# Optimization experiments

Measured on AMD Instinct MI355X. Metric: run time of the kernel, lower is better.

Reference implementation:

```python
import jax, jax.numpy as jnp
import numpy as np

SEQ = 4096
STATE_DIM = 512
ACTION_DIM = 496
T_DIM = 16
EMBED = STATE_DIM + ACTION_DIM + T_DIM  # 1024
HEADS = 4
HEAD_DIM = EMBED // HEADS
FF = 4096
N_EXP = 8
TOP_K = 2
EPS = 1e-5


def _ln(x, g, b):
    m = jnp.mean(x, -1, keepdims=True)
    v = jnp.var(x, -1, keepdims=True)
    return (x - m) * jax.lax.rsqrt(v + EPS) * g + b


def setup_inputs() -> dict:
    key = jax.random.key(0)
    ks = jax.random.split(key, 24)
    s = lambda k, shape, scale=0.02: jax.random.normal(k, shape, dtype=jnp.float32) * scale
    return {
        "x": jax.random.normal(ks[0], (SEQ, ACTION_DIM), dtype=jnp.float32),
        "time": jax.random.randint(ks[1], (SEQ,), 0, 6),
        "state": jax.random.normal(ks[2], (SEQ, 1, STATE_DIM), dtype=jnp.float32),
        "time_table": s(ks[3], (6, T_DIM), 1.0),
        "expert_w": s(ks[4], (N_EXP, EMBED, EMBED)),   # [n, in, out]
        "expert_b": jnp.zeros((N_EXP, EMBED), jnp.float32),
        "gate_w": s(ks[5], (EMBED, N_EXP)),
        "gate_b": jnp.zeros((N_EXP,), jnp.float32),
        "in_proj_w": s(ks[6], (EMBED, 3 * EMBED)),
        "in_proj_b": jnp.zeros((3 * EMBED,), jnp.float32),
        "out_proj_w": s(ks[7], (EMBED, EMBED)),
        "out_proj_b": jnp.zeros((EMBED,), jnp.float32),
        "ln1_g": jnp.ones((EMBED,), jnp.float32),
        "ln1_b": jnp.zeros((EMBED,), jnp.float32),
        "ff1_w": s(ks[8], (EMBED, FF)),
        "ff1_b": jnp.zeros((FF,), jnp.float32),
        "ff2_w": s(ks[9], (FF, ACTION_DIM)),
        "ff2_b": jnp.zeros((ACTION_DIM,), jnp.float32),
        "ln2_g": jnp.ones((ACTION_DIM,), jnp.float32),
        "ln2_b": jnp.zeros((ACTION_DIM,), jnp.float32),
    }


def reference(x, time, state, time_table, expert_w, expert_b, gate_w, gate_b,
              in_proj_w, in_proj_b, out_proj_w, out_proj_b,
              ln1_g, ln1_b, ff1_w, ff1_b, ff2_w, ff2_b, ln2_g, ln2_b):
    # combine inputs -> [S, EMBED]
    t_emb = time_table[time]                      # [S, t_dim]
    h = jnp.concatenate([x, t_emb, state[:, 0, :]], axis=-1)

    # MoE: softmax gate, top-k combine over densely-computed expert outputs
    gate = jax.nn.softmax(h @ gate_w + gate_b, axis=-1)      # [S, N]
    scores, idx = jax.lax.top_k(gate, TOP_K)                 # [S, K]
    all_out = jnp.einsum('se,nef->snf', h, expert_w) + expert_b[None]  # [S, N, E]
    comb = jnp.zeros_like(gate).at[jnp.arange(SEQ)[:, None], idx].add(scores)
    moe = jnp.einsum('sn,snf->sf', comb, all_out)            # [S, E]

    # multi-head self-attention (torch nn.MultiheadAttention, unbatched)
    qkv = moe @ in_proj_w + in_proj_b
    q, k, v = jnp.split(qkv, 3, axis=-1)
    q = q.reshape(SEQ, HEADS, HEAD_DIM) * (HEAD_DIM ** -0.5)
    k = k.reshape(SEQ, HEADS, HEAD_DIM)
    v = v.reshape(SEQ, HEADS, HEAD_DIM)
    att = jax.nn.softmax(jnp.einsum('shd,thd->hst', q, k), axis=-1)
    ao = jnp.einsum('hst,thd->shd', att, v).reshape(SEQ, EMBED)
    ao = ao @ out_proj_w + out_proj_b

    out1 = _ln(moe + ao, ln1_g, ln1_b)
    ff = jax.nn.relu(out1 @ ff1_w + ff1_b) @ ff2_w + ff2_b   # [S, action_dim]
    return _ln(ff, ln2_g, ln2_b)
```

## Files before the change

kernel.cpp:

```cpp
#include <hip/hip_runtime.h>
#include <hip/hip_bf16.h>

typedef __hip_bfloat16 hb;
typedef __bf16 bf16x8 __attribute__((ext_vector_type(8)));
typedef float f32x4 __attribute__((ext_vector_type(4)));

#define SEQ 4096
#define EMBED 1024
#define NHEAD 4
#define HDIM 256
#define FFD 4096
#define NEXP 8
#define ADIM 496
#define NSLOT 9216

static __device__ __forceinline__ float b2f(hb x) { return __bfloat162float(x); }
static __device__ __forceinline__ hb f2b(float x) { return __float2bfloat16(x); }

#define GLOAD_LDS16(g, l)                                                      \
  __builtin_amdgcn_global_load_lds(                                            \
      (const __attribute__((address_space(1))) void*)(g),                      \
      (__attribute__((address_space(3))) void*)(l), 16, 0, 0)

#define GEMM_KLOOP64(KMAX)                                                     \
  for (int kt = 0; kt < (KMAX); kt += 64) {                                    \
    GLOAD_LDS16(Ag + kt, sA + wave * 512);                                     \
    GLOAD_LDS16(Ag + kt + 32, sA + 4096 + wave * 512);                         \
    GLOAD_LDS16(Ag + kt + 64 * lda_, sA + 2048 + wave * 512);                  \
    GLOAD_LDS16(Ag + kt + 64 * lda_ + 32, sA + 6144 + wave * 512);             \
    GLOAD_LDS16(Bg + kt, sB + wave * 512);                                     \
    GLOAD_LDS16(Bg + kt + 32, sB + 4096 + wave * 512);                         \
    GLOAD_LDS16(Bg + kt + 64 * ldb_, sB + 2048 + wave * 512);                  \
    GLOAD_LDS16(Bg + kt + 64 * ldb_ + 32, sB + 6144 + wave * 512);             \
    __syncthreads();                                                           \
    _Pragma("unroll") for (int ks = 0; ks < 2; ks++) {                         \
      bf16x8 av[4], bv[4];                                                     \
      _Pragma("unroll") for (int i = 0; i < 4; i++) {                          \
        const int row = wr * 64 + i * 16 + lm;                                 \
        av[i] = *(const bf16x8*)&sA[ks * 4096 + row * 32 + sw8];               \
      }                                                                        \
      _Pragma("unroll") for (int i = 0; i < 4; i++) {                          \
        const int row = wc * 64 + i * 16 + lm;                                 \
        bv[i] = *(const bf16x8*)&sB[ks * 4096 + row * 32 + sw8];               \
      }                                                                        \
      _Pragma("unroll") for (int i = 0; i < 4; i++)                            \
          _Pragma("unroll") for (int j = 0; j < 4; j++) acc[i][j] =            \
          __builtin_amdgcn_mfma_f32_16x16x32_bf16(av[i], bv[j], acc[i][j], 0,  \
                                                  0, 0);                       \
    }                                                                          \
    __syncthreads();                                                           \
  }

#define GEMM_PROLOGUE                                                          \
  const int m0 = blockIdx.y * 128, n0 = blockIdx.x * 128;                      \
  const int tid = threadIdx.x;                                                 \
  const int wave = tid >> 6, lane = tid & 63;                                  \
  const int quad = lane >> 4, lm = lane & 15;                                  \
  const int wr = wave >> 1, wc = wave & 1;                                     \
  const int r0 = tid >> 2;                                                     \
  const int cg = 8 * ((tid & 3) ^ ((tid >> 2) & 3));                           \
  const int sw8 = (quad ^ (lm & 3)) * 8;

#define EPILOGUE_B16(DST, LDC)                                                 \
  {                                                                            \
    hb* eb = smem + wave * 1024;                                               \
    _Pragma("unroll") for (int i = 0; i < 4; i++) {                            \
      _Pragma("unroll") for (int j = 0; j < 4; j++) {                          \
        const int c = ((j ^ quad) << 4) + lm;                                  \
        _Pragma("unroll") for (int rr = 0; rr < 4; rr++)                       \
            eb[(quad * 4 + rr) * 64 + c] = f2b(acc[i][j][rr]);                 \
      }                                                                        \
      _Pragma("unroll") for (int p = 0; p < 2; p++) {                          \
        const int r = p * 8 + (lane >> 3);                                     \
        const int cgc = lane & 7;                                              \
        const int gs = (cgc >> 1) ^ (r >> 2);                                  \
        const bf16x8 val =                                                     \
            *(const bf16x8*)&eb[r * 64 + gs * 16 + (cgc & 1) * 8];             \
        const long grow = m0 + wr * 64 + i * 16 + r;                           \
        *(bf16x8*)&DST[grow * (LDC) + n0 + wc * 64 + cgc * 8] = val;           \
      }                                                                        \
    }                                                                          \
  }

__global__ __launch_bounds__(256) void gemm_bt(
    const hb* __restrict__ A, long lda, long bA,
    const hb* __restrict__ B, long ldb, long bB,
    hb* __restrict__ C, long ldc, long bC,
    int K, const float* __restrict__ bias, int relu) {
  __shared__ __align__(16) hb smem[2 * 128 * 64];
  hb* sA = smem;
  hb* sB = smem + 8192;
  const int z = blockIdx.z;
  A += (long)z * bA;
  B += (long)z * bB;
  C += (long)z * bC;
  GEMM_PROLOGUE
  const long lda_ = lda, ldb_ = ldb;
  const hb* Ag = A + (long)(m0 + r0) * lda + cg;
  const hb* Bg = B + (long)(n0 + r0) * ldb + cg;

  f32x4 acc[4][4] = {};
  GEMM_KLOOP64(K)

  hb* eb = smem + wave * 1024;
#pragma unroll
  for (int i = 0; i < 4; i++) {
#pragma unroll
    for (int j = 0; j < 4; j++) {
      const float bval = bias ? bias[n0 + wc * 64 + j * 16 + lm] : 0.f;
      const int c = ((j ^ quad) << 4) + lm;
#pragma unroll
      for (int rr = 0; rr < 4; rr++) {
        float v = acc[i][j][rr] + bval;
        if (relu) v = fmaxf(v, 0.f);
        eb[(quad * 4 + rr) * 64 + c] = f2b(v);
      }
    }
#pragma unroll
    for (int p = 0; p < 2; p++) {
      const int r = p * 8 + (lane >> 3);
      const int cgc = lane & 7;
      const int gs = (cgc >> 1) ^ (r >> 2);
      const bf16x8 val = *(const bf16x8*)&eb[r * 64 + gs * 16 + (cgc & 1) * 8];
      const long grow = m0 + wr * 64 + i * 16 + r;
      *(bf16x8*)&C[grow * ldc + n0 + wc * 64 + cgc * 8] = val;
    }
  }
}

__global__ __launch_bounds__(256) void gemm_bt_exp(
    const hb* __restrict__ A, long lda, long bA,
    const hb* __restrict__ B, long ldb, long bB,
    hb* __restrict__ C, long ldc, long bC,
    int K, float scale, hb* __restrict__ rsP) {
  __shared__ __align__(16) hb smem[2 * 128 * 64];
  hb* sA = smem;
  hb* sB = smem + 8192;
  const int z = blockIdx.z;
  A += (long)z * bA;
  B += (long)z * bB;
  C += (long)z * bC;
  GEMM_PROLOGUE
  const long lda_ = lda, ldb_ = ldb;
  const hb* Ag = A + (long)(m0 + r0) * lda + cg;
  const hb* Bg = B + (long)(n0 + r0) * ldb + cg;

  f32x4 acc[4][4] = {};
  GEMM_KLOOP64(K)

  hb* eb = smem + wave * 1024;
  float* rbuf = (float*)sB;
  float rs[4][4];
#pragma unroll
  for (int i = 0; i < 4; i++) {
    float r4[4] = {0.f, 0.f, 0.f, 0.f};
#pragma unroll
    for (int j = 0; j < 4; j++) {
      const int c = ((j ^ quad) << 4) + lm;
#pragma unroll
      for (int rr = 0; rr < 4; rr++) {
        const float e = __expf(acc[i][j][rr] * scale);
        r4[rr] += e;
        eb[(quad * 4 + rr) * 64 + c] = f2b(e);
      }
    }
#pragma unroll
    for (int rr = 0; rr < 4; rr++) {
      r4[rr] += __shfl_xor(r4[rr], 1);
      r4[rr] += __shfl_xor(r4[rr], 2);
      r4[rr] += __shfl_xor(r4[rr], 4);
      r4[rr] += __shfl_xor(r4[rr], 8);
      rs[i][rr] = r4[rr];
    }
#pragma unroll
    for (int p = 0; p < 2; p++) {
      const int r = p * 8 + (lane >> 3);
      const int cgc = lane & 7;
      const int gs = (cgc >> 1) ^ (r >> 2);
      const bf16x8 val = *(const bf16x8*)&eb[r * 64 + gs * 16 + (cgc & 1) * 8];
      const long grow = m0 + wr * 64 + i * 16 + r;
      *(bf16x8*)&C[grow * ldc + n0 + wc * 64 + cgc * 8] = val;
    }
  }
  if (lm == 0) {
#pragma unroll
    for (int i = 0; i < 4; i++)
#pragma unroll
      for (int rr = 0; rr < 4; rr++)
        rbuf[(wr * 2 + wc) * 64 + i * 16 + quad * 4 + rr] = rs[i][rr];
  }
  __syncthreads();
  if (tid < 128) {
    const int lwr = tid >> 6, r64 = tid & 63;
    const float d = rbuf[lwr * 128 + r64] + rbuf[lwr * 128 + 64 + r64];
    rsP[((long)blockIdx.x * gridDim.z + z) * SEQ + m0 + lwr * 64 + r64] =
        f2b(d);
  }
}

__global__ __launch_bounds__(256) void gemm_bt_splitk(
    const hb* __restrict__ A, long lda, long bA,
    const hb* __restrict__ B, long ldb, long bB,
    float* __restrict__ Cp, int ldcp, long pstride, int Ksub, int shift) {
  const int z = blockIdx.z;
  const int batch = z >> shift, split = z - (batch << shift);
  A += (long)batch * bA + (long)split * Ksub;
  B += (long)batch * bB + (long)split * Ksub;
  Cp += (long)z * pstride;
  __shared__ __align__(16) hb smem[2 * 128 * 64];
  hb* sA = smem;
  hb* sB = smem + 8192;
  GEMM_PROLOGUE
  const long lda_ = lda, ldb_ = ldb;
  const hb* Ag = A + (long)(m0 + r0) * lda + cg;
  const hb* Bg = B + (long)(n0 + r0) * ldb + cg;

  f32x4 acc[4][4] = {};
  GEMM_KLOOP64(Ksub)

  float* ef = (float*)smem + wave * 1024;
#pragma unroll
  for (int i = 0; i < 4; i++) {
#pragma unroll
    for (int j = 0; j < 4; j++) {
      const int c = ((j ^ quad) << 4) + lm;
#pragma unroll
      for (int rr = 0; rr < 4; rr++)
        ef[(quad * 4 + rr) * 64 + c] = acc[i][j][rr];
    }
#pragma unroll
    for (int p = 0; p < 4; p++) {
      const int r = p * 4 + (lane >> 4);
      const int cgc = lane & 15;
      const int gs = (cgc >> 2) ^ (r >> 2);
      const f32x4 val = *(const f32x4*)&ef[r * 64 + gs * 16 + (cgc & 3) * 4];
      const long grow = m0 + wr * 64 + i * 16 + r;
      *(f32x4*)&Cp[grow * ldcp + n0 + wc * 64 + cgc * 4] = val;
    }
  }
}

__global__ __launch_bounds__(256) void gemm_bt_splitk_b16(
    const hb* __restrict__ A, long lda, long bA,
    const hb* __restrict__ B, long ldb, long bB,
    hb* __restrict__ Cp, int ldcp, long pstride, int Ksub, int shift) {
  const int z = blockIdx.z;
  const int batch = z >> shift, split = z - (batch << shift);
  A += (long)batch * bA + (long)split * Ksub;
  B += (long)batch * bB + (long)split * Ksub;
  Cp += (long)z * pstride;
  __shared__ __align__(16) hb smem[2 * 128 * 64];
  hb* sA = smem;
  hb* sB = smem + 8192;
  GEMM_PROLOGUE
  const long lda_ = lda, ldb_ = ldb;
  const hb* Ag = A + (long)(m0 + r0) * lda + cg;
  const hb* Bg = B + (long)(n0 + r0) * ldb + cg;

  f32x4 acc[4][4] = {};
  GEMM_KLOOP64(Ksub)
  EPILOGUE_B16(Cp, ldcp)
}

__global__ __launch_bounds__(256) void reduce_splitk(
    const float* __restrict__ part, long pstride, int nsplit, int shift,
    hb* __restrict__ C, long ldc, long bC, int Nshift) {
  const long idx = (long)blockIdx.x * 256 + threadIdx.x;
  const int batch = blockIdx.y;
  float v = 0.f;
  for (int k = 0; k < nsplit; k++)
    v += part[(long)((batch << shift) + k) * pstride + idx];
  const long row = idx >> Nshift;
  const long col = idx & ((1 << Nshift) - 1);
  C[(long)batch * bC + row * ldc + col] = f2b(v);
}

__global__ __launch_bounds__(256) void reduce_pv(
    const hb* __restrict__ part, const hb* __restrict__ rsP,
    hb* __restrict__ ao) {
  const int row = blockIdx.x, head = blockIdx.y, tid = threadIdx.x;
  __shared__ float dsh;
  if (tid < 64) {
    float p = b2f(rsP[((long)(tid & 31) * NHEAD + head) * SEQ + row]);
#pragma unroll
    for (int o = 32; o; o >>= 1) p += __shfl_down(p, o);
    if (tid == 0) dsh = 0.5f * p;
  }
  __syncthreads();
  const float den = dsh;
  const long base = ((long)(head * 2) * SEQ + row) * 256 + tid;
  const float v = b2f(part[base]) + b2f(part[base + (long)SEQ * 256]);
  ao[(long)row * 1024 + head * 256 + tid] = f2b(v / den);
}

__global__ __launch_bounds__(256) void gemm_moe(
    const hb* __restrict__ h, const hb* __restrict__ expertT,
    const int* __restrict__ slot_token, const int* __restrict__ eblk,
    hb* __restrict__ slotout) {
  const int e = eblk[blockIdx.y];
  if (e < 0) return;
  __shared__ __align__(16) hb smem[2 * 128 * 64];
  hb* sA = smem;
  hb* sB = smem + 8192;
  GEMM_PROLOGUE
  const int t0 = slot_token[m0 + r0];
  const int t1 = slot_token[m0 + r0 + 64];
  const hb* B = expertT + ((long)e << 20);
  const hb* Ag0 = h + (long)t0 * EMBED + cg;
  const hb* Ag1 = h + (long)t1 * EMBED + cg;
  const hb* Bg = B + (long)(n0 + r0) * EMBED + cg;

  f32x4 acc[4][4] = {};
  for (int kt = 0; kt < EMBED; kt += 64) {
    GLOAD_LDS16(Ag0 + kt, sA + wave * 512);
    GLOAD_LDS16(Ag0 + kt + 32, sA + 4096 + wave * 512);
    GLOAD_LDS16(Ag1 + kt, sA + 2048 + wave * 512);
    GLOAD_LDS16(Ag1 + kt + 32, sA + 6144 + wave * 512);
    GLOAD_LDS16(Bg + kt, sB + wave * 512);
    GLOAD_LDS16(Bg + kt + 32, sB + 4096 + wave * 512);
    GLOAD_LDS16(Bg + kt + 64 * EMBED, sB + 2048 + wave * 512);
    GLOAD_LDS16(Bg + kt + 64 * EMBED + 32, sB + 6144 + wave * 512);
    __syncthreads();
#pragma unroll
    for (int ks = 0; ks < 2; ks++) {
      bf16x8 av[4], bv[4];
#pragma unroll
      for (int i = 0; i < 4; i++) {
        const int row = wr * 64 + i * 16 + lm;
        av[i] = *(const bf16x8*)&sA[ks * 4096 + row * 32 + sw8];
      }
#pragma unroll
      for (int i = 0; i < 4; i++) {
        const int row = wc * 64 + i * 16 + lm;
        bv[i] = *(const bf16x8*)&sB[ks * 4096 + row * 32 + sw8];
      }
#pragma unroll
      for (int i = 0; i < 4; i++)
#pragma unroll
        for (int j = 0; j < 4; j++)
          acc[i][j] = __builtin_amdgcn_mfma_f32_16x16x32_bf16(av[i], bv[j],
                                                              acc[i][j], 0, 0, 0);
    }
    __syncthreads();
  }
  EPILOGUE_B16(slotout, EMBED)
}

__global__ __launch_bounds__(256) void transpose_all(
    const float* __restrict__ expert_w, const float* __restrict__ in_proj_w,
    const float* __restrict__ out_proj_w, const float* __restrict__ ff1_w,
    const float* __restrict__ ff2_w, hb* __restrict__ expertT,
    hb* __restrict__ inprojT, hb* __restrict__ outprojT, hb* __restrict__ ff1T,
    hb* __restrict__ ff2T) {
  const int b = blockIdx.x;
  const float* in;
  hb* outp;
  int R, Cin, Cout, ldin, ldout, bx, by;
  if (b < 8192) {
    const int z = b >> 10, l = b & 1023;
    bx = l & 31; by = l >> 5;
    in = expert_w + (long)z * 1048576; outp = expertT + (long)z * 1048576;
    R = 1024; Cin = 1024; Cout = 1024; ldin = 1024; ldout = 1024;
  } else if (b < 11264) {
    const int l = b - 8192;
    bx = l % 96; by = l / 96;
    in = in_proj_w; outp = inprojT;
    R = 1024; Cin = 3072; Cout = 3072; ldin = 3072; ldout = 1024;
  } else if (b < 12288) {
    const int l = b - 11264;
    bx = l & 31; by = l >> 5;
    in = out_proj_w; outp = outprojT;
    R = 1024; Cin = 1024; Cout = 1024; ldin = 1024; ldout = 1024;
  } else if (b < 16384) {
    const int l = b - 12288;
    bx = l & 127; by = l >> 7;
    in = ff1_w; outp = ff1T;
    R = 1024; Cin = 4096; Cout = 4096; ldin = 4096; ldout = 1024;
  } else {
    const int l = b - 16384;
    bx = l & 15; by = l >> 4;
    in = ff2_w; outp = ff2T;
    R = 4096; Cin = 496; Cout = 512; ldin = 496; ldout = 4096;
  }
  __shared__ hb tile[32][33];
  const int c0 = bx * 32, r0 = by * 32;
  const int tx = threadIdx.x, ty = threadIdx.y;
#pragma unroll
  for (int i = 0; i < 32; i += 8) {
    const int r = r0 + ty + i, c = c0 + tx;
    hb v = f2b(0.f);
    if (r < R && c < Cin) v = f2b(in[(long)r * ldin + c]);
    tile[ty + i][tx] = v;
  }
  __syncthreads();
#pragma unroll
  for (int i = 0; i < 32; i += 8) {
    const int c = c0 + ty + i, r = r0 + tx;
    if (c < Cout && r < R) outp[(long)c * ldout + r] = tile[tx][ty + i];
  }
}

__global__ __launch_bounds__(256) void transpose_v(
    const hb* __restrict__ in, hb* __restrict__ out) {
  __shared__ hb tile[32][33];
  const int z = blockIdx.z;
  in += (long)z * 256;
  out += (long)z * 1048576;
  const int c0 = blockIdx.x * 32, r0 = blockIdx.y * 32;
  const int tx = threadIdx.x, ty = threadIdx.y;
#pragma unroll
  for (int i = 0; i < 32; i += 8)
    tile[ty + i][tx] = in[(long)(r0 + ty + i) * 3072 + c0 + tx];
  __syncthreads();
#pragma unroll
  for (int i = 0; i < 32; i += 8)
    out[(long)(c0 + ty + i) * 4096 + r0 + tx] = tile[tx][ty + i];
}

__global__ __launch_bounds__(256) void bh_gate_kernel(
    const float* __restrict__ x, const int* __restrict__ timev,
    const float* __restrict__ state, const float* __restrict__ ttab,
    const float* __restrict__ gw, const float* __restrict__ gb,
    hb* __restrict__ h, int* __restrict__ tok_e, float* __restrict__ tok_w) {
  const int s = blockIdx.x, tid = threadIdx.x;
  const int wv = tid >> 6, ln = tid & 63;
  const int t = timev[s];
  float acc[8] = {0, 0, 0, 0, 0, 0, 0, 0};
  for (int c = tid; c < EMBED; c += 256) {
    float v;
    if (c < ADIM)
      v = x[(long)s * ADIM + c];
    else if (c < ADIM + 16)
      v = ttab[t * 16 + (c - ADIM)];
    else
      v = state[(long)s * 512 + (c - 512)];
    h[(long)s * EMBED + c] = f2b(v);
    const float* g = gw + c * 8;
#pragma unroll
    for (int n = 0; n < 8; n++) acc[n] += v * g[n];
  }
#pragma unroll
  for (int o = 32; o; o >>= 1)
#pragma unroll
    for (int n = 0; n < 8; n++) acc[n] += __shfl_down(acc[n], o);
  __shared__ float red[4][8];
  if (ln == 0)
#pragma unroll
    for (int n = 0; n < 8; n++) red[wv][n] = acc[n];
  __syncthreads();
  if (tid == 0) {
    float lg[8], m = -1e30f;
    for (int n = 0; n < 8; n++) {
      lg[n] = red[0][n] + red[1][n] + red[2][n] + red[3][n] + gb[n];
      m = fmaxf(m, lg[n]);
    }
    float den = 0.f;
    for (int n = 0; n < 8; n++) {
      lg[n] = expf(lg[n] - m);
      den += lg[n];
    }
    for (int n = 0; n < 8; n++) lg[n] /= den;
    int i1 = 0;
    for (int n = 1; n < 8; n++)
      if (lg[n] > lg[i1]) i1 = n;
    int i2 = (i1 == 0) ? 1 : 0;
    for (int n = 0; n < 8; n++) {
      if (n == i1) continue;
      if (lg[n] > lg[i2]) i2 = n;
    }
    tok_e[2 * s] = i1;
    tok_w[2 * s] = lg[i1];
    tok_e[2 * s + 1] = i2;
    tok_w[2 * s + 1] = lg[i2];
  }
}

__global__ __launch_bounds__(256) void group_kernel(
    const int* __restrict__ tok_e, int* __restrict__ slot_token,
    int* __restrict__ token_slot, int* __restrict__ eblk) {
  __shared__ int cnt[8], off[9], cur[8];
  const int tid = threadIdx.x;
  if (tid < 8) cnt[tid] = 0;
  for (int i = tid; i < NSLOT; i += 256) slot_token[i] = 0;
  __syncthreads();
  for (int i = tid; i < 2 * SEQ; i += 256) atomicAdd(&cnt[tok_e[i]], 1);
  __syncthreads();
  if (tid == 0) {
    int o = 0;
    for (int n = 0; n < 8; n++) {
      off[n] = o;
      cur[n] = o;
      o += (cnt[n] + 127) & ~127;
    }
    off[8] = o;
  }
  __syncthreads();
  if (tid < NSLOT / 128) {
    const int rb = tid * 128;
    int e = -1;
    for (int n = 0; n < 8; n++)
      if (rb >= off[n] && rb < off[n + 1]) e = n;
    eblk[tid] = e;
  }
  for (int i = tid; i < 2 * SEQ; i += 256) {
    const int e = tok_e[i];
    const int slot = atomicAdd(&cur[e], 1);
    slot_token[slot] = i >> 1;
    token_slot[i] = slot;
  }
}

__global__ __launch_bounds__(256) void moe_combine_kernel(
    const hb* __restrict__ slotout, const int* __restrict__ token_slot,
    const float* __restrict__ tok_w, const int* __restrict__ tok_e,
    const float* __restrict__ eb, hb* __restrict__ moe) {
  const int s = blockIdx.x, tid = threadIdx.x;
  const int s0 = token_slot[2 * s], s1 = token_slot[2 * s + 1];
  const float w0 = tok_w[2 * s], w1 = tok_w[2 * s + 1];
  const int e0 = tok_e[2 * s], e1 = tok_e[2 * s + 1];
  const hb* r0 = slotout + (long)s0 * EMBED;
  const hb* r1 = slotout + (long)s1 * EMBED;
  const float* b0 = eb + e0 * EMBED;
  const float* b1 = eb + e1 * EMBED;
  for (int c = tid; c < EMBED; c += 256) {
    const float v = w0 * (b2f(r0[c]) + b0[c]) + w1 * (b2f(r1[c]) + b1[c]);
    moe[(long)s * EMBED + c] = f2b(v);
  }
}

__global__ __launch_bounds__(256) void softmax_fast(hb* __restrict__ S,
                                                    float scale) {
  const long row = blockIdx.x;
  const int tid = threadIdx.x, wv = tid >> 6, ln = tid & 63;
  hb* p = S + row * 4096 + tid * 16;
  __shared__ float red[4];
  bf16x8 a0 = *(const bf16x8*)p;
  bf16x8 a1 = *(const bf16x8*)(p + 8);
  float v[16];
#pragma unroll
  for (int i = 0; i < 8; i++) {
    v[i] = (float)a0[i];
    v[8 + i] = (float)a1[i];
  }
  float m = v[0];
#pragma unroll
  for (int i = 1; i < 16; i++) m = fmaxf(m, v[i]);
#pragma unroll
  for (int o = 32; o; o >>= 1) m = fmaxf(m, __shfl_down(m, o));
  if (ln == 0) red[wv] = m;
  __syncthreads();
  const float M = fmaxf(fmaxf(red[0], red[1]), fmaxf(red[2], red[3])) * scale;
  __syncthreads();
  float sum = 0.f;
#pragma unroll
  for (int i = 0; i < 16; i++) {
    v[i] = __expf(v[i] * scale - M);
    sum += v[i];
  }
#pragma unroll
  for (int o = 32; o; o >>= 1) sum += __shfl_down(sum, o);
  if (ln == 0) red[wv] = sum;
  __syncthreads();
  const float inv = 1.f / (red[0] + red[1] + red[2] + red[3]);
#pragma unroll
  for (int i = 0; i < 8; i++) {
    a0[i] = (__bf16)(v[i] * inv);
    a1[i] = (__bf16)(v[8 + i] * inv);
  }
  *(bf16x8*)p = a0;
  *(bf16x8*)(p + 8) = a1;
}

__global__ __launch_bounds__(256) void ln_kernel(
    const hb* __restrict__ in, long ldin, const hb* __restrict__ resid,
    long ldr, const float* __restrict__ g, const float* __restrict__ beta,
    hb* __restrict__ outb, long ldout, int ncol) {
  const int s = blockIdx.x, tid = threadIdx.x, wv = tid >> 6, ln = tid & 63;
  __shared__ float buf[1024];
  __shared__ float red[4];
  float sum = 0.f, sq = 0.f;
  for (int c = tid; c < ncol; c += 256) {
    float v = b2f(in[(long)s * ldin + c]);
    if (resid) v += b2f(resid[(long)s * ldr + c]);
    buf[c] = v;
    sum += v;
    sq += v * v;
  }
#pragma unroll
  for (int o = 32; o; o >>= 1) sum += __shfl_down(sum, o);
  if (ln == 0) red[wv] = sum;
  __syncthreads();
  const float S = red[0] + red[1] + red[2] + red[3];
  __syncthreads();
#pragma unroll
  for (int o = 32; o; o >>= 1) sq += __shfl_down(sq, o);
  if (ln == 0) red[wv] = sq;
  __syncthreads();
  const float Q = red[0] + red[1] + red[2] + red[3];
  const float mean = S / ncol;
  const float var = Q / ncol - mean * mean;
  const float r = rsqrtf(var + 1e-5f);
  for (int c = tid; c < ncol; c += 256)
    outb[(long)s * ldout + c] = f2b((buf[c] - mean) * r * g[c] + beta[c]);
}

__global__ __launch_bounds__(256) void ln2_red_kernel(
    const float* __restrict__ part, long pstride,
    const float* __restrict__ bias, const float* __restrict__ g,
    const float* __restrict__ beta, float* __restrict__ out) {
  const int s = blockIdx.x, tid = threadIdx.x, wv = tid >> 6, ln = tid & 63;
  __shared__ float buf[512];
  __shared__ float red[4];
  float sum = 0.f, sq = 0.f;
  for (int c = tid; c < ADIM; c += 256) {
    const long idx = (long)s * 512 + c;
    float v = part[idx] + part[pstride + idx] + part[2 * pstride + idx] +
              part[3 * pstride + idx] + bias[c];
    buf[c] = v;
    sum += v;
    sq += v * v;
  }
#pragma unroll
  for (int o = 32; o; o >>= 1) sum += __shfl_down(sum, o);
  if (ln == 0) red[wv] = sum;
  __syncthreads();
  const float S = red[0] + red[1] + red[2] + red[3];
  __syncthreads();
#pragma unroll
  for (int o = 32; o; o >>= 1) sq += __shfl_down(sq, o);
  if (ln == 0) red[wv] = sq;
  __syncthreads();
  const float Q = red[0] + red[1] + red[2] + red[3];
  const float mean = S / ADIM;
  const float var = Q / ADIM - mean * mean;
  const float r = rsqrtf(var + 1e-5f);
  for (int c = tid; c < ADIM; c += 256)
    out[(long)s * ADIM + c] = (buf[c] - mean) * r * g[c] + beta[c];
}

__global__ __launch_bounds__(256) void ln2_red_b16_kernel(
    const hb* __restrict__ part, long pstride,
    const float* __restrict__ bias, const float* __restrict__ g,
    const float* __restrict__ beta, float* __restrict__ out) {
  const int s = blockIdx.x, tid = threadIdx.x, wv = tid >> 6, ln = tid & 63;
  __shared__ float buf[512];
  __shared__ float red[4];
  float sum = 0.f, sq = 0.f;
  for (int c = tid; c < ADIM; c += 256) {
    const long idx = (long)s * 512 + c;
    float v = b2f(part[idx]) + b2f(part[pstride + idx]) +
              b2f(part[2 * pstride + idx]) + b2f(part[3 * pstride + idx]) +
              bias[c];
    buf[c] = v;
    sum += v;
    sq += v * v;
  }
#pragma unroll
  for (int o = 32; o; o >>= 1) sum += __shfl_down(sum, o);
  if (ln == 0) red[wv] = sum;
  __syncthreads();
  const float S = red[0] + red[1] + red[2] + red[3];
  __syncthreads();
#pragma unroll
  for (int o = 32; o; o >>= 1) sq += __shfl_down(sq, o);
  if (ln == 0) red[wv] = sq;
  __syncthreads();
  const float Q = red[0] + red[1] + red[2] + red[3];
  const float mean = S / ADIM;
  const float var = Q / ADIM - mean * mean;
  const float r = rsqrtf(var + 1e-5f);
  for (int c = tid; c < ADIM; c += 256)
    out[(long)s * ADIM + c] = (buf[c] - mean) * r * g[c] + beta[c];
}

extern "C" void kernel_launch(void* const* d_in, const int* in_sizes, int n_in,
                              void* d_out, int out_size, void* d_ws,
                              size_t ws_size, hipStream_t stream) {
  const float* x = (const float*)d_in[0];
  const int* timev = (const int*)d_in[1];
  const float* state = (const float*)d_in[2];
  const float* ttab = (const float*)d_in[3];
  const float* expert_w = (const float*)d_in[4];
  const float* expert_b = (const float*)d_in[5];
  const float* gate_w = (const float*)d_in[6];
  const float* gate_b = (const float*)d_in[7];
  const float* in_proj_w = (const float*)d_in[8];
  const float* in_proj_b = (const float*)d_in[9];
  const float* out_proj_w = (const float*)d_in[10];
  const float* out_proj_b = (const float*)d_in[11];
  const float* ln1_g = (const float*)d_in[12];
  const float* ln1_b = (const float*)d_in[13];
  const float* ff1_w = (const float*)d_in[14];
  const float* ff1_b = (const float*)d_in[15];
  const float* ff2_w = (const float*)d_in[16];
  const float* ff2_b = (const float*)d_in[17];
  const float* ln2_g = (const float*)d_in[18];
  const float* ln2_b = (const float*)d_in[19];
  float* out = (float*)d_out;

  char* w = (char*)d_ws;
  const long MB = 1048576;
  const bool big = ws_size >= (size_t)(192 * MB);

  hb* expertT = (hb*)(w + 0 * MB);
  hb* slotout = (hb*)(w + 16 * MB);
  hb* h = (hb*)(w + 35 * MB);
  hb* inprojT = (hb*)(w + 43 * MB);
  hb* outprojT = (hb*)(w + (big ? 168 : 49) * MB);
  hb* ff1T = (hb*)(w + (big ? 170 : 51) * MB);
  hb* ff2T = (hb*)(w + (big ? 178 : 59) * MB);
  const long metaOff = (big ? 190 : 63) * MB;
  int* tok_e = (int*)(w + metaOff);
  float* tok_w = (float*)(w + metaOff + 32768);
  int* slot_token = (int*)(w + metaOff + 65536);
  int* token_slot = (int*)(w + metaOff + 102400);
  int* eblk = (int*)(w + metaOff + 135168);
  hb* rsP = (hb*)(w + metaOff + 163840);
  hb* moe = (hb*)(w + (big ? 152 : 64) * MB);
  hb* qkv = (hb*)(w + (big ? 0 : 72) * MB);
  hb* scores = (hb*)(w + (big ? 24 : 96) * MB);
  hb* vt = (hb*)(w + (big ? 160 : 8) * MB);
  hb* ao = (hb*)(w + (big ? 182 : 0) * MB);
  hb* ao2 = (hb*)(w + (big ? 24 : 8) * MB);
  hb* out1 = (hb*)(w + (big ? 32 : 132) * MB);
  hb* ffmid = (hb*)(w + (big ? 40 : 96) * MB);
  float* part = (float*)(w + (big ? 72 : 16) * MB);
  hb* partb16 = (hb*)(w + (big ? 72 : 16) * MB);
  hb* pvpart = (hb*)(w + 0 * MB);
  (void)in_sizes; (void)n_in; (void)out_size;

  transpose_all<<<dim3(18432), dim3(32, 8), 0, stream>>>(
      expert_w, in_proj_w, out_proj_w, ff1_w, ff2_w, expertT, inprojT, outprojT,
      ff1T, ff2T);

  bh_gate_kernel<<<dim3(SEQ), 256, 0, stream>>>(x, timev, state, ttab, gate_w,
                                                gate_b, h, tok_e, tok_w);
  group_kernel<<<dim3(1), 256, 0, stream>>>(tok_e, slot_token, token_slot, eblk);

  gemm_moe<<<dim3(8, NSLOT / 128), 256, 0, stream>>>(h, expertT, slot_token,
                                                     eblk, slotout);
  moe_combine_kernel<<<dim3(SEQ), 256, 0, stream>>>(slotout, token_slot, tok_w,
                                                    tok_e, expert_b, moe);

  gemm_bt<<<dim3(24, 32, 1), 256, 0, stream>>>(moe, 1024, 0, inprojT, 1024, 0,
                                               qkv, 3072, 0, 1024, in_proj_b, 0);
  transpose_v<<<dim3(8, 128, 4), dim3(32, 8), 0, stream>>>(qkv + 2048, vt);

  if (big) {
    gemm_bt_exp<<<dim3(32, 32, 4), 256, 0, stream>>>(
        qkv, 3072, 256, qkv + 1024, 3072, 256, scores, 4096, (long)SEQ * SEQ,
        HDIM, 0.0625f, rsP);
    gemm_bt_splitk_b16<<<dim3(2, 32, 8), 256, 0, stream>>>(
        scores, 4096, (long)SEQ * SEQ, vt, 4096, 1048576L, pvpart, 256,
        (long)SEQ * 256, 2048, 1);
    reduce_pv<<<dim3(4096, 4), 256, 0, stream>>>(pvpart, rsP, ao);
  } else {
    for (int hp = 0; hp < 2; ++hp) {
      const hb* qb = qkv + hp * 512;
      const hb* kb = qkv + 1024 + hp * 512;
      gemm_bt<<<dim3(32, 32, 2), 256, 0, stream>>>(
          qb, 3072, 256, kb, 3072, 256, scores, 4096, (long)SEQ * SEQ, HDIM,
          nullptr, 0);
      softmax_fast<<<dim3(2 * SEQ), 256, 0, stream>>>(scores, 0.0625f);
      gemm_bt_splitk<<<dim3(2, 32, 8), 256, 0, stream>>>(
          scores, 4096, (long)SEQ * SEQ, vt + (long)hp * 2097152, 4096,
          1048576L, part, 256, (long)SEQ * 256, 1024, 2);
      reduce_splitk<<<dim3(4096, 2), 256, 0, stream>>>(
          part, (long)SEQ * 256, 4, 2, ao + hp * 512, 1024, 256, 8);
    }
  }

  gemm_bt<<<dim3(8, 32, 1), 256, 0, stream>>>(ao, 1024, 0, outprojT, 1024, 0,
                                              ao2, 1024, 0, 1024, out_proj_b, 0);
  ln_kernel<<<dim3(SEQ), 256, 0, stream>>>(moe, 1024, ao2, 1024, ln1_g, ln1_b,
                                           out1, 1024, 1024);

  gemm_bt<<<dim3(32, 32, 1), 256, 0, stream>>>(out1, 1024, 0, ff1T, 1024, 0,
                                               ffmid, 4096, 0, 1024, ff1_b, 1);
  if (big) {
    gemm_bt_splitk_b16<<<dim3(4, 32, 4), 256, 0, stream>>>(
        ffmid, 4096, 0, ff2T, 4096, 0, partb16, 512, (long)SEQ * 512, 1024, 2);
    ln2_red_b16_kernel<<<dim3(SEQ), 256, 0, stream>>>(
        partb16, (long)SEQ * 512, ff2_b, ln2_g, ln2_b, out);
  } else {
    gemm_bt_splitk<<<dim3(4, 32, 4), 256, 0, stream>>>(
        ffmid, 4096, 0, ff2T, 4096, 0, part, 512, (long)SEQ * 512, 1024, 2);
    ln2_red_kernel<<<dim3(SEQ), 256, 0, stream>>>(part, (long)SEQ * 512, ff2_b,
                                                  ln2_g, ln2_b, out);
  }
}
```

Baseline: 530.7 us.

## Store attention probabilities and V in FP8 and use FP8 MFMA for PV

The exp-scores GEMM now writes unnormalized probabilities as e4m3 FP8 instead of bf16, which halves the 4x4096x4096 score matrix traffic. V is transposed into FP8, and a new split-K PV kernel uses the fp8 16x16x32 MFMA with 8-bit LDS tiles. The intent is to cut the memory traffic and matrix time of the attention PV stage. Unnormalized exp values can reach large magnitudes and e4m3 has coarse precision, so accuracy may drop.

```diff
diff --git a/kernel.cpp b/kernel.cpp
--- a/kernel.cpp
+++ b/kernel.cpp
@@ -1,5 +1,6 @@
 #include <hip/hip_runtime.h>
 #include <hip/hip_bf16.h>
+#include <hip/hip_fp8.h>
 
 typedef __hip_bfloat16 hb;
 typedef __bf16 bf16x8 __attribute__((ext_vector_type(8)));
@@ -16,6 +17,10 @@
 
 static __device__ __forceinline__ float b2f(hb x) { return __bfloat162float(x); }
 static __device__ __forceinline__ hb f2b(float x) { return __float2bfloat16(x); }
+static __device__ __forceinline__ unsigned char f2e4m3(float v) {
+  __hip_fp8_e4m3 t(v);
+  return t.__x;
+}
 
 #define GLOAD_LDS16(g, l)                                                      \
   __builtin_amdgcn_global_load_lds(                                            \
@@ -131,7 +136,7 @@
 __global__ __launch_bounds__(256) void gemm_bt_exp(
     const hb* __restrict__ A, long lda, long bA,
     const hb* __restrict__ B, long ldb, long bB,
-    hb* __restrict__ C, long ldc, long bC,
+    unsigned char* __restrict__ C, long ldc, long bC,
     int K, float scale, hb* __restrict__ rsP) {
   __shared__ __align__(16) hb smem[2 * 128 * 64];
   hb* sA = smem;
@@ -148,7 +153,7 @@
   f32x4 acc[4][4] = {};
   GEMM_KLOOP64(K)
 
-  hb* eb = smem + wave * 1024;
+  unsigned char* eb8 = (unsigned char*)smem + wave * 1024;
   float* rbuf = (float*)sB;
   float rs[4][4];
 #pragma unroll
@@ -161,7 +166,7 @@
       for (int rr = 0; rr < 4; rr++) {
         const float e = __expf(acc[i][j][rr] * scale);
         r4[rr] += e;
-        eb[(quad * 4 + rr) * 64 + c] = f2b(e);
+        eb8[(quad * 4 + rr) * 64 + c] = f2e4m3(e);
       }
     }
 #pragma unroll
@@ -172,14 +177,13 @@
       r4[rr] += __shfl_xor(r4[rr], 8);
       rs[i][rr] = r4[rr];
     }
-#pragma unroll
-    for (int p = 0; p < 2; p++) {
-      const int r = p * 8 + (lane >> 3);
-      const int cgc = lane & 7;
-      const int gs = (cgc >> 1) ^ (r >> 2);
-      const bf16x8 val = *(const bf16x8*)&eb[r * 64 + gs * 16 + (cgc & 1) * 8];
+    {
+      const int r = lane >> 2;
+      const int cgc = lane & 3;
+      const f32x4 val =
+          *(const f32x4*)&eb8[r * 64 + ((cgc ^ (r >> 2)) << 4)];
       const long grow = m0 + wr * 64 + i * 16 + r;
-      *(bf16x8*)&C[grow * ldc + n0 + wc * 64 + cgc * 8] = val;
+      *(f32x4*)&C[grow * ldc + n0 + wc * 64 + cgc * 16] = val;
     }
   }
   if (lm == 0) {
@@ -196,6 +200,64 @@
     rsP[((long)blockIdx.x * gridDim.z + z) * SEQ + m0 + lwr * 64 + r64] =
         f2b(d);
   }
+}
+
+__global__ __launch_bounds__(256) void pv_f8_splitk(
+    const unsigned char* __restrict__ S, const unsigned char* __restrict__ Vt,
+    hb* __restrict__ Cp) {
+  const int z = blockIdx.z;
+  const int head = z >> 1, split = z & 1;
+  const unsigned char* A = S + (long)head * SEQ * SEQ + split * 2048;
+  const unsigned char* B = Vt + ((long)head << 20) + split * 2048;
+  hb* Cb = Cp + (long)z * SEQ * 256;
+  __shared__ __align__(16) unsigned char smem8[16384];
+  hb* smem = (hb*)smem8;
+  unsigned char* sA8 = smem8;
+  unsigned char* sB8 = smem8 + 8192;
+  const int m0 = blockIdx.y * 128, n0 = blockIdx.x * 128;
+  const int tid = threadIdx.x;
+  const int wave = tid >> 6, lane = tid & 63;
+  const int quad = lane >> 4, lm = lane & 15;
+  const int wr = wave >> 1, wc = wave & 1;
+  const int r8 = tid >> 2;
+  const int cg8 = 16 * ((tid & 3) ^ (r8 & 3));
+  const unsigned char* Ag = A + (long)(m0 + r8) * 4096 + cg8;
+  const unsigned char* Bg = B + (long)(n0 + r8) * 4096 + cg8;
+
+  f32x4 acc[4][4] = {};
+  for (int kt = 0; kt < 2048; kt += 64) {
+    GLOAD_LDS16(Ag + kt, sA8 + wave * 1024);
+    GLOAD_LDS16(Ag + kt + 64 * 4096, sA8 + 4096 + wave * 1024);
+    GLOAD_LDS16(Bg + kt, sB8 + wave * 1024);
+    GLOAD_LDS16(Bg + kt + 64 * 4096, sB8 + 4096 + wave * 1024);
+    __syncthreads();
+#pragma unroll
+    for (int ks = 0; ks < 2; ks++) {
+      long a8[4], b8[4];
+#pragma unroll
+      for (int i = 0; i < 4; i++) {
+        const int row = wr * 64 + i * 16 + lm;
+        a8[i] = *(const long*)&sA8[row * 64 +
+                                   (((ks * 2 + (quad >> 1)) ^ (row & 3)) << 4) +
+                                   (quad & 1) * 8];
+      }
+#pragma unroll
+      for (int i = 0; i < 4; i++) {
+        const int row = wc * 64 + i * 16 + lm;
+        b8[i] = *(const long*)&sB8[row * 64 +
+                                   (((ks * 2 + (quad >> 1)) ^ (row & 3)) << 4) +
+                                   (quad & 1) * 8];
+      }
+#pragma unroll
+      for (int i = 0; i < 4; i++)
+#pragma unroll
+        for (int j = 0; j < 4; j++)
+          acc[i][j] = __builtin_amdgcn_mfma_f32_16x16x32_fp8_fp8(
+              a8[i], b8[j], acc[i][j], 0, 0, 0);
+    }
+    __syncthreads();
+  }
+  EPILOGUE_B16(Cb, 256)
 }
 
 __global__ __launch_bounds__(256) void gemm_bt_splitk(
@@ -417,6 +479,23 @@
     out[(long)(c0 + ty + i) * 4096 + r0 + tx] = tile[tx][ty + i];
 }
 
+__global__ __launch_bounds__(256) void transpose_v8(
+    const hb* __restrict__ in, unsigned char* __restrict__ out) {
+  __shared__ hb tile[32][33];
+  const int z = blockIdx.z;
+  in += (long)z * 256;
+  out += (long)z * 1048576;
+  const int c0 = blockIdx.x * 32, r0 = blockIdx.y * 32;
+  const int tx = threadIdx.x, ty = threadIdx.y;
+#pragma unroll
+  for (int i = 0; i < 32; i += 8)
+    tile[ty + i][tx] = in[(long)(r0 + ty + i) * 3072 + c0 + tx];
+  __syncthreads();
+#pragma unroll
+  for (int i = 0; i < 32; i += 8)
+    out[(long)(c0 + ty + i) * 4096 + r0 + tx] = f2e4m3(b2f(tile[tx][ty + i]));
+}
+
 __global__ __launch_bounds__(256) void bh_gate_kernel(
     const float* __restrict__ x, const int* __restrict__ timev,
     const float* __restrict__ state, const float* __restrict__ ttab,
@@ -718,8 +797,10 @@
   hb* rsP = (hb*)(w + metaOff + 163840);
   hb* moe = (hb*)(w + (big ? 152 : 64) * MB);
   hb* qkv = (hb*)(w + (big ? 0 : 72) * MB);
-  hb* scores = (hb*)(w + (big ? 24 : 96) * MB);
-  hb* vt = (hb*)(w + (big ? 160 : 8) * MB);
+  unsigned char* scores8 = (unsigned char*)(w + 24 * MB);
+  hb* scores = (hb*)(w + 96 * MB);
+  unsigned char* vt8 = (unsigned char*)(w + 160 * MB);
+  hb* vt = (hb*)(w + 8 * MB);
   hb* ao = (hb*)(w + (big ? 182 : 0) * MB);
   hb* ao2 = (hb*)(w + (big ? 24 : 8) * MB);
   hb* out1 = (hb*)(w + (big ? 32 : 132) * MB);
@@ -744,15 +825,16 @@
 
   gemm_bt<<<dim3(24, 32, 1), 256, 0, stream>>>(moe, 1024, 0, inprojT, 1024, 0,
                                                qkv, 3072, 0, 1024, in_proj_b, 0);
-  transpose_v<<<dim3(8, 128, 4), dim3(32, 8), 0, stream>>>(qkv + 2048, vt);
+  if (big)
+    transpose_v8<<<dim3(8, 128, 4), dim3(32, 8), 0, stream>>>(qkv + 2048, vt8);
+  else
+    transpose_v<<<dim3(8, 128, 4), dim3(32, 8), 0, stream>>>(qkv + 2048, vt);
 
   if (big) {
     gemm_bt_exp<<<dim3(32, 32, 4), 256, 0, stream>>>(
-        qkv, 3072, 256, qkv + 1024, 3072, 256, scores, 4096, (long)SEQ * SEQ,
+        qkv, 3072, 256, qkv + 1024, 3072, 256, scores8, 4096, (long)SEQ * SEQ,
         HDIM, 0.0625f, rsP);
-    gemm_bt_splitk_b16<<<dim3(2, 32, 8), 256, 0, stream>>>(
-        scores, 4096, (long)SEQ * SEQ, vt, 4096, 1048576L, pvpart, 256,
-        (long)SEQ * 256, 2048, 1);
+    pv_f8_splitk<<<dim3(2, 32, 8), 256, 0, stream>>>(scores8, vt8, pvpart);
     reduce_pv<<<dim3(4096, 4), 256, 0, stream>>>(pvpart, rsP, ao);
   } else {
     for (int hp = 0; hp < 2; ++hp) {
```

Result: no change. 536.8 us (+1.1%).
